# Optimization experiments

Hardware: AMD Instinct MI355X
Metric: run time of the kernel (lower is better)

Reference implementation:

```python
import jax, jax.numpy as jnp
import numpy as np

N, E, D, H, K, G = 100000, 1600000, 64, 64, 3, 64


def setup_inputs() -> dict:
    key = jax.random.key(0)
    ks = jax.random.split(key, 16)
    x = jax.random.normal(ks[0], (N, D), dtype=jnp.float32)
    edge_index = jax.random.randint(ks[1], (2, E), 0, N, dtype=jnp.int64)
    batch = jnp.sort(jax.random.randint(ks[2], (N,), 0, G, dtype=jnp.int64))
    s = 0.1
    inp = {
        "x": x, "edge_index": edge_index, "batch": batch,
        # ChebConv weights: [K, Din, Dout] and bias [Dout]
        "w1": jax.random.normal(ks[3], (K, D, H), dtype=jnp.float32) * s,
        "b1": jnp.zeros((H,), jnp.float32),
        "w2": jax.random.normal(ks[4], (K, H, H), dtype=jnp.float32) * s,
        "b2": jnp.zeros((H,), jnp.float32),
        "w3": jax.random.normal(ks[5], (K, H, H), dtype=jnp.float32) * s,
        "b3": jnp.zeros((H,), jnp.float32),
        # BatchNorm affine params
        "g1": jnp.ones((H,), jnp.float32), "be1": jnp.zeros((H,), jnp.float32),
        "g2": jnp.ones((H,), jnp.float32), "be2": jnp.zeros((H,), jnp.float32),
        "g3": jnp.ones((H,), jnp.float32), "be3": jnp.zeros((H,), jnp.float32),
        # shortcut Linear(input_dim, hidden3) and lin1(hidden3, 1)
        "w_sc": jax.random.normal(ks[6], (D, H), dtype=jnp.float32) * s,
        "b_sc": jnp.zeros((H,), jnp.float32),
        "w_lin": jax.random.normal(ks[7], (H, 1), dtype=jnp.float32) * s,
        "b_lin": jnp.zeros((1,), jnp.float32),
    }
    return inp


def _laplacian_norm(row, col, n):
    # PyG ChebConv default: sym normalization, lambda_max=2 -> L_hat = L - I = -D^{-1/2} A D^{-1/2}
    deg = jax.ops.segment_sum(jnp.ones(row.shape[0], jnp.float32), row, num_segments=n)
    dis = jnp.where(deg > 0, jax.lax.rsqrt(jnp.maximum(deg, 1e-12)), 0.0)
    return -dis[row] * dis[col]  # [E]


def _cheb_conv(x, row, col, norm, W, b):
    n = x.shape[0]
    prop = lambda z: jax.ops.segment_sum(norm[:, None] * z[col], row, num_segments=n)
    Tx0 = x
    out = Tx0 @ W[0]
    Tx1 = prop(Tx0)
    out = out + Tx1 @ W[1]
    for k in range(2, W.shape[0]):
        Tx2 = 2.0 * prop(Tx1) - Tx0
        out = out + Tx2 @ W[k]
        Tx0, Tx1 = Tx1, Tx2
    return out + b


def _bn(x, g, b, eps=1e-5):
    mu = jnp.mean(x, axis=0)
    var = jnp.mean(jnp.square(x - mu), axis=0)  # biased, as torch BN training stats
    return (x - mu) * jax.lax.rsqrt(var + eps) * g + b


def reference(x, edge_index, batch, w1, b1, w2, b2, w3, b3,
              g1, be1, g2, be2, g3, be3, w_sc, b_sc, w_lin, b_lin):
    row, col = edge_index[0], edge_index[1]
    norm = _laplacian_norm(row, col, x.shape[0])
    lrelu = lambda h: jax.nn.leaky_relu(h, negative_slope=0.01)
    identity = x
    h = lrelu(_bn(_cheb_conv(x, row, col, norm, w1, b1), g1, be1))
    h = lrelu(_bn(_cheb_conv(h, row, col, norm, w2, b2), g2, be2))
    h = lrelu(_bn(_cheb_conv(h, row, col, norm, w3, b3), g3, be3))
    h = h + (identity @ w_sc + b_sc)
    pooled = jax.ops.segment_max(h, batch, num_segments=G)  # [G, H]
    return pooled @ w_lin + b_lin  # [G, 1]
```

## Files before the change

### kernel.cpp

```cpp
#include <hip/hip_runtime.h>

#define DIV_UP(a,b) (((a)+(b)-1)/(b))

typedef float v4f __attribute__((ext_vector_type(4)));
typedef unsigned short us4 __attribute__((ext_vector_type(4)));
typedef __attribute__((ext_vector_type(8))) short bf16x8;
typedef __attribute__((ext_vector_type(4))) float f32x4;

__device__ __forceinline__ float4 ntload4(const float* p) {
  v4f v = __builtin_nontemporal_load((const v4f*)p);
  return make_float4(v.x, v.y, v.z, v.w);
}

__device__ __forceinline__ unsigned f2key(float f) {
  unsigned u = __float_as_uint(f);
  return (u & 0x80000000u) ? ~u : (u | 0x80000000u);
}
__device__ __forceinline__ float key2f(unsigned u) {
  unsigned b = (u & 0x80000000u) ? (u ^ 0x80000000u) : ~u;
  return __uint_as_float(b);
}

__device__ __forceinline__ unsigned short f2bf(float f) {
  unsigned u = __float_as_uint(f);
  unsigned r = u + 0x7FFFu + ((u >> 16) & 1u);
  return (unsigned short)(r >> 16);
}
__device__ __forceinline__ float bf2f(unsigned short s) {
  return __uint_as_float(((unsigned)s) << 16);
}

__global__ void k_scan1(const int* __restrict__ cnt, int* __restrict__ incl,
                        int* __restrict__ bsum, int N) {
  __shared__ int s[1024];
  int t = threadIdx.x;
  int i = blockIdx.x * 1024 + t;
  int v = (i < N) ? cnt[i] : 0;
  s[t] = v;
  __syncthreads();
  for (int off = 1; off < 1024; off <<= 1) {
    int add = (t >= off) ? s[t - off] : 0;
    __syncthreads();
    s[t] += add;
    __syncthreads();
  }
  if (i < N) incl[i] = s[t];
  if (t == 1023) bsum[blockIdx.x] = s[1023];
}

__global__ void k_scan2(const int* __restrict__ bsum, int* __restrict__ bex, int nb) {
  __shared__ int s[128];
  int t = threadIdx.x;
  if (nb <= 128) {
    int v = (t < nb) ? bsum[t] : 0;
    s[t] = v;
    __syncthreads();
    for (int off = 1; off < 128; off <<= 1) {
      int add = (t >= off) ? s[t - off] : 0;
      __syncthreads();
      s[t] += add;
      __syncthreads();
    }
    if (t < nb) bex[t] = s[t] - v;
  } else if (t == 0) {
    int run = 0;
    for (int b = 0; b < nb; ++b) { bex[b] = run; run += bsum[b]; }
  }
}

__global__ void k_scan3(const int* __restrict__ incl, const int* __restrict__ cnt,
                        const int* __restrict__ bex, int* __restrict__ rowptr,
                        int* __restrict__ cursor, float* __restrict__ dis,
                        int N, int E) {
  int i = blockIdx.x * blockDim.x + threadIdx.x;
  if (i < N) {
    int c = cnt[i];
    int v = incl[i] - c + bex[i >> 10];
    rowptr[i] = v;
    cursor[i] = v;
    dis[i] = (c > 0) ? rsqrtf((float)c) : 0.0f;
  }
  if (i == 0) rowptr[N] = E;
}

__device__ __forceinline__ void gemmsc_body(unsigned short* wTsc, unsigned short* x16,
                                            int bid,
                                            const float* __restrict__ X,
                                            const float* __restrict__ W,
                                            const float* __restrict__ bias,
                                            unsigned short* __restrict__ Sbf, int N) {
  int tid = threadIdx.x;
  for (int i4 = tid; i4 < 1024; i4 += 512) {
    int d = i4 >> 4, h4 = i4 & 15;
    float4 v = ((const float4*)W)[i4];
    int colb = h4 * 4;
    wTsc[(colb + 0) * 64 + d] = f2bf(v.x);
    wTsc[(colb + 1) * 64 + d] = f2bf(v.y);
    wTsc[(colb + 2) * 64 + d] = f2bf(v.z);
    wTsc[(colb + 3) * 64 + d] = f2bf(v.w);
  }
  int rowbase = bid * 128;
  for (int i4 = tid; i4 < 2048; i4 += 512) {
    int r = i4 >> 4, c4 = i4 & 15;
    int row = rowbase + r;
    float4 v = (row < N) ? ntload4(X + (size_t)row * 64 + c4 * 4)
                         : make_float4(0.f, 0.f, 0.f, 0.f);
    us4 pk;
    pk.x = f2bf(v.x); pk.y = f2bf(v.y); pk.z = f2bf(v.z); pk.w = f2bf(v.w);
    *(us4*)&x16[r * 64 + c4 * 4] = pk;
  }
  __syncthreads();

  int lane = tid & 63;
  int wv = tid >> 6;
  int lo = lane & 15;
  int hi = lane >> 4;

  f32x4 acc[4];
#pragma unroll
  for (int ct = 0; ct < 4; ++ct) acc[ct] = (f32x4){0.f, 0.f, 0.f, 0.f};

#pragma unroll
  for (int ks = 0; ks < 2; ++ks) {
    bf16x8 af = *(const bf16x8*)&x16[(wv * 16 + lo) * 64 + ks * 32 + hi * 8];
#pragma unroll
    for (int ct = 0; ct < 4; ++ct) {
      bf16x8 bfr = *(const bf16x8*)&wTsc[(ct * 16 + lo) * 64 + ks * 32 + hi * 8];
      acc[ct] = __builtin_amdgcn_mfma_f32_16x16x32_bf16(af, bfr, acc[ct], 0, 0, 0);
    }
  }

  float bv[4];
#pragma unroll
  for (int ct = 0; ct < 4; ++ct) bv[ct] = bias[ct * 16 + lo];
  int rowb = rowbase + wv * 16 + hi * 4;
#pragma unroll
  for (int reg = 0; reg < 4; ++reg) {
    int row = rowb + reg;
    if (row < N) {
      size_t o = (size_t)row * 64 + lo;
#pragma unroll
      for (int ct = 0; ct < 4; ++ct)
        __builtin_nontemporal_store(f2bf(acc[ct][reg] + bv[ct]), &Sbf[o + ct * 16]);
    }
  }
}

__device__ __forceinline__ void mfma192_tail(const unsigned short* x16,
                                             const unsigned short* wT,
                                             int rowbase, int tid,
                                             const float* __restrict__ bias,
                                             const float* __restrict__ dis,
                                             unsigned short* __restrict__ A02bf,
                                             unsigned short* __restrict__ Y1bf,
                                             unsigned short* __restrict__ Y2bf,
                                             int N) {
  int lane = tid & 63;
  int wv = tid >> 6;
  int lo = lane & 15;
  int hi = lane >> 4;

  f32x4 acc[12];
#pragma unroll
  for (int ct = 0; ct < 12; ++ct) acc[ct] = (f32x4){0.f, 0.f, 0.f, 0.f};

#pragma unroll
  for (int ks = 0; ks < 2; ++ks) {
    bf16x8 af = *(const bf16x8*)&x16[(wv * 16 + lo) * 64 + ks * 32 + hi * 8];
#pragma unroll
    for (int ct = 0; ct < 12; ++ct) {
      bf16x8 bfr = *(const bf16x8*)&wT[(ct * 16 + lo) * 64 + ks * 32 + hi * 8];
      acc[ct] = __builtin_amdgcn_mfma_f32_16x16x32_bf16(af, bfr, acc[ct], 0, 0, 0);
    }
  }

  float bv[4];
#pragma unroll
  for (int ct = 0; ct < 4; ++ct) bv[ct] = bias[ct * 16 + lo];
  int rowb = rowbase + wv * 16 + hi * 4;
#pragma unroll
  for (int reg = 0; reg < 4; ++reg) {
    int row = rowb + reg;
    if (row < N) {
      float dn = dis[row];
      size_t o = (size_t)row * 64 + lo;
#pragma unroll
      for (int ct = 0; ct < 4; ++ct) {
        float o0 = acc[ct][reg] + bv[ct];
        float o1 = acc[ct + 4][reg];
        float o2 = acc[ct + 8][reg];
        A02bf[o + ct * 16] = f2bf(o0 - o2);
        Y1bf[o + ct * 16] = f2bf(o1);
        Y2bf[o + ct * 16] = f2bf(dn * o2);
      }
    }
  }
}

__device__ __forceinline__ void stage_wT(unsigned short* wT,
                                         const float* __restrict__ W, int tid) {
  for (int i4 = tid; i4 < 3072; i4 += 512) {
    int k3 = i4 >> 10, rem = i4 & 1023;
    int d = rem >> 4, h4 = rem & 15;
    float4 v = ((const float4*)W)[i4];
    int colb = k3 * 64 + h4 * 4;
    wT[(colb + 0) * 64 + d] = f2bf(v.x);
    wT[(colb + 1) * 64 + d] = f2bf(v.y);
    wT[(colb + 2) * 64 + d] = f2bf(v.z);
    wT[(colb + 3) * 64 + d] = f2bf(v.w);
  }
}

__device__ __forceinline__ void gemm192_l0_body(unsigned short* x16, unsigned short* wT,
                                                int bid,
                                                const float* __restrict__ X,
                                                const float* __restrict__ W,
                                                const float* __restrict__ bias,
                                                const float* __restrict__ dis,
                                                unsigned short* __restrict__ A02bf,
                                                unsigned short* __restrict__ Y1bf,
                                                unsigned short* __restrict__ Y2bf,
                                                int N) {
  int tid = threadIdx.x;
  stage_wT(wT, W, tid);
  int rowbase = bid * 128;
  for (int i4 = tid; i4 < 2048; i4 += 512) {
    int r = i4 >> 4, c4 = i4 & 15;
    int row = rowbase + r;
    float4 v = (row < N) ? ntload4(X + (size_t)row * 64 + c4 * 4)
                         : make_float4(0.f, 0.f, 0.f, 0.f);
    us4 pk;
    pk.x = f2bf(v.x); pk.y = f2bf(v.y); pk.z = f2bf(v.z); pk.w = f2bf(v.w);
    *(us4*)&x16[r * 64 + c4 * 4] = pk;
  }
  __syncthreads();
  mfma192_tail(x16, wT, rowbase, tid, bias, dis, A02bf, Y1bf, Y2bf, N);
}

__global__ __launch_bounds__(512) void k_fused_a(const float* __restrict__ X,
                                                 const float* __restrict__ W,
                                                 const float* __restrict__ bias,
                                                 unsigned short* __restrict__ Sbf,
                                                 const int* __restrict__ row,
                                                 int* __restrict__ cnt,
                                                 unsigned short* __restrict__ Y2bf,
                                                 unsigned short* __restrict__ Vbf,
                                                 unsigned* __restrict__ pooled,
                                                 int N, int E, int NBG, int NC,
                                                 int npool, int q) {
  __shared__ unsigned short wTsc[64 * 64];
  __shared__ unsigned short x16a[128 * 64];
  int bid = blockIdx.x;
  bool isg = (bid % q == 0) && (bid / q < NBG);
  if (isg) {
    gemmsc_body(wTsc, x16a, bid / q, X, W, bias, Sbf, N);
  } else {
    int before = min((bid + q - 1) / q, NBG);
    int oi = bid - before;
    if (oi < NC) {
      int e0 = oi * 2048 + threadIdx.x;
      int r[4];
#pragma unroll
      for (int k = 0; k < 4; ++k) {
        int e = e0 + k * 512;
        if (e < E) r[k] = row[e];
      }
#pragma unroll
      for (int k = 0; k < 4; ++k) {
        int e = e0 + k * 512;
        if (e < E) atomicAdd(&cnt[r[k]], 1);
      }
    } else if (oi == NC) {
      if (threadIdx.x < 64) {
        Y2bf[(size_t)N * 64 + threadIdx.x] = 0;
        Vbf[(size_t)N * 64 + threadIdx.x] = 0;
      }
    } else {
      int i = (oi - NC - 1) * 512 + threadIdx.x;
      if (i < npool) pooled[i] = 0x007FFFFFu;
    }
  }
}

__global__ __launch_bounds__(512) void k_fused_b(const float* __restrict__ X,
                                                 const float* __restrict__ W,
                                                 const float* __restrict__ bias,
                                                 const float* __restrict__ dis,
                                                 unsigned short* __restrict__ A02bf,
                                                 unsigned short* __restrict__ Y1bf,
                                                 unsigned short* __restrict__ Y2bf,
                                                 const int* __restrict__ row,
                                                 const int* __restrict__ col,
                                                 int* __restrict__ cursor,
                                                 int* __restrict__ ccol,
                                                 int N, int E, int NBG, int q) {
  __shared__ unsigned short x16b[128 * 64];
  __shared__ unsigned short wTb[192 * 64];
  int bid = blockIdx.x;
  bool isg = (bid % q == 0) && (bid / q < NBG);
  if (isg) {
    gemm192_l0_body(x16b, wTb, bid / q, X, W, bias, dis, A02bf, Y1bf, Y2bf, N);
  } else {
    int before = min((bid + q - 1) / q, NBG);
    int oi = bid - before;
    int e0 = oi * 2048 + threadIdx.x;
    int r[4], c[4], idx[4];
#pragma unroll
    for (int k = 0; k < 4; ++k) {
      int e = e0 + k * 512;
      if (e < E) { r[k] = row[e]; c[k] = col[e]; }
    }
#pragma unroll
    for (int k = 0; k < 4; ++k) {
      int e = e0 + k * 512;
      if (e < E) idx[k] = atomicAdd(&cursor[r[k]], 1);
    }
#pragma unroll
    for (int k = 0; k < 4; ++k) {
      int e = e0 + k * 512;
      if (e < E) ccol[idx[k]] = c[k];
    }
  }
}

__global__ __launch_bounds__(512) void k_gemm192(
    const unsigned short* __restrict__ Cbf,
    const float* __restrict__ sums, const float* __restrict__ sumsq,
    const float* __restrict__ g, const float* __restrict__ be,
    const float* __restrict__ W, const float* __restrict__ bias,
    const float* __restrict__ dis,
    unsigned short* __restrict__ A02bf, unsigned short* __restrict__ Y1bf,
    unsigned short* __restrict__ Y2bf, int N) {
  __shared__ unsigned short x16[128 * 64];
  __shared__ unsigned short wT[192 * 64];
  int bid = blockIdx.x;
  int tid = threadIdx.x;

  int cb = (tid & 15) * 4;
  float inv_n = 1.0f / (float)N;
  float scv[4], shv[4];
#pragma unroll
  for (int k = 0; k < 4; ++k) {
    float mu = sums[cb + k] * inv_n;
    float var = sumsq[cb + k] * inv_n - mu * mu;
    float sc = g[cb + k] * rsqrtf(var + 1e-5f);
    scv[k] = sc;
    shv[k] = be[cb + k] - mu * sc;
  }

  stage_wT(wT, W, tid);

  int rowbase = bid * 128;
  for (int i4 = tid; i4 < 2048; i4 += 512) {
    int r = i4 >> 4, c4 = i4 & 15;
    int row = rowbase + r;
    float vx, vy, vz, vw;
    if (row < N) {
      unsigned long long u =
          *(const unsigned long long*)(Cbf + (size_t)row * 64 + c4 * 4);
      vx = bf2f((unsigned short)(u & 0xffffu));
      vy = bf2f((unsigned short)((u >> 16) & 0xffffu));
      vz = bf2f((unsigned short)((u >> 32) & 0xffffu));
      vw = bf2f((unsigned short)(u >> 48));
    } else {
      vx = vy = vz = vw = 0.f;
    }
    float a = vx * scv[0] + shv[0];
    float b = vy * scv[1] + shv[1];
    float c = vz * scv[2] + shv[2];
    float d = vw * scv[3] + shv[3];
    a = (a > 0.f) ? a : 0.01f * a;
    b = (b > 0.f) ? b : 0.01f * b;
    c = (c > 0.f) ? c : 0.01f * c;
    d = (d > 0.f) ? d : 0.01f * d;
    us4 pk;
    pk.x = f2bf(a); pk.y = f2bf(b); pk.z = f2bf(c); pk.w = f2bf(d);
    *(us4*)&x16[r * 64 + c4 * 4] = pk;
  }
  __syncthreads();

  mfma192_tail(x16, wT, rowbase, tid, bias, dis, A02bf, Y1bf, Y2bf, N);
}

__device__ __forceinline__ void gather4(int cw, int qtr, int s,
                                        const unsigned long long* z64, float* a) {
#pragma unroll
  for (int u = 0; u < 4; ++u) {
    int c = __shfl(cw, 4 * u + qtr, 64);
    unsigned long long zv = z64[(size_t)c * 16 + s];
    unsigned d0 = (unsigned)zv, d1 = (unsigned)(zv >> 32);
    a[0] += __uint_as_float(d0 << 16);
    a[1] += __uint_as_float(d0 & 0xFFFF0000u);
    a[2] += __uint_as_float(d1 << 16);
    a[3] += __uint_as_float(d1 & 0xFFFF0000u);
  }
}

template <int MODE>
__global__ __launch_bounds__(256) void k_prop4(const int* __restrict__ rowptr,
                                               const int* __restrict__ ccol,
                                               const float* __restrict__ dis,
                                               const unsigned short* __restrict__ zbf,
                                               const unsigned short* __restrict__ inAbf,
                                               unsigned short* __restrict__ outbf,
                                               float* __restrict__ sums,
                                               float* __restrict__ sumsq,
                                               float* __restrict__ zstats,
                                               int N, int nwaves) {
  if (MODE == 1 && blockIdx.x == 0 && threadIdx.x < 128) zstats[threadIdx.x] = 0.f;
  int gw = blockIdx.x * 4 + (threadIdx.x >> 6);
  int lane = threadIdx.x & 63;
  int wid = threadIdx.x >> 6;
  int qtr = lane >> 4;
  int s = lane & 15;
  const unsigned long long* z64 = (const unsigned long long*)zbf;
  const unsigned long long* inA64 = (const unsigned long long*)inAbf;
  unsigned long long* out64 = (unsigned long long*)outbf;
  float st[4] = {0.f, 0.f, 0.f, 0.f}, st2[4] = {0.f, 0.f, 0.f, 0.f};

  int n = gw, beg = 0, end = 0, cl = 0;
  if (n < N) {
    beg = rowptr[n];
    end = rowptr[n + 1];
    cl = ccol[beg + s];
  }
  while (n < N) {
    int nn = n + nwaves;
    int begn = 0, endn = 0;
    if (nn < N) {
      begn = rowptr[nn];
      endn = rowptr[nn + 1];
    }
    float dn = dis[n];
    size_t o = (size_t)n * 16 + s;
    unsigned long long av = 0;
    if (qtr == 0) av = inA64[o];
    float a[4] = {0.f, 0.f, 0.f, 0.f};
    {
      int c16 = (beg + s < end) ? cl : N;
      gather4(c16, qtr, s, z64, a);
    }
    for (int j = beg + 16; j < end; j += 16) {
      int jj = j + s;
      int c = ccol[jj];
      c = (jj < end) ? c : N;
      gather4(c, qtr, s, z64, a);
    }
    int cln = 0;
    if (nn < N) cln = ccol[begn + s];
#pragma unroll
    for (int k = 0; k < 4; ++k) {
      a[k] += __shfl_xor(a[k], 16, 64);
      a[k] += __shfl_xor(a[k], 32, 64);
    }
    if (qtr == 0) {
      unsigned b0 = (unsigned)av, b1 = (unsigned)(av >> 32);
      float x0 = __uint_as_float(b0 << 16);
      float x1 = __uint_as_float(b0 & 0xFFFF0000u);
      float x2 = __uint_as_float(b1 << 16);
      float x3 = __uint_as_float(b1 & 0xFFFF0000u);
      if (MODE == 1) {
        float v0 = dn * (x0 - 2.f * dn * a[0]);
        float v1 = dn * (x1 - 2.f * dn * a[1]);
        float v2 = dn * (x2 - 2.f * dn * a[2]);
        float v3 = dn * (x3 - 2.f * dn * a[3]);
        unsigned lo = (unsigned)f2bf(v0) | ((unsigned)f2bf(v1) << 16);
        unsigned hi = (unsigned)f2bf(v2) | ((unsigned)f2bf(v3) << 16);
        out64[o] = (unsigned long long)lo | ((unsigned long long)hi << 32);
      } else {
        float v0 = x0 - dn * a[0];
        float v1 = x1 - dn * a[1];
        float v2 = x2 - dn * a[2];
        float v3 = x3 - dn * a[3];
        unsigned lo = (unsigned)f2bf(v0) | ((unsigned)f2bf(v1) << 16);
        unsigned hi = (unsigned)f2bf(v2) | ((unsigned)f2bf(v3) << 16);
        out64[o] = (unsigned long long)lo | ((unsigned long long)hi << 32);
        st[0] += v0; st2[0] = fmaf(v0, v0, st2[0]);
        st[1] += v1; st2[1] = fmaf(v1, v1, st2[1]);
        st[2] += v2; st2[2] = fmaf(v2, v2, st2[2]);
        st[3] += v3; st2[3] = fmaf(v3, v3, st2[3]);
      }
    }
    n = nn; beg = begn; end = endn; cl = cln;
  }
  if (MODE == 2) {
    __shared__ float red[2][4][64];
    if (qtr == 0) {
#pragma unroll
      for (int k = 0; k < 4; ++k) {
        red[0][wid][4 * s + k] = st[k];
        red[1][wid][4 * s + k] = st2[k];
      }
    }
    __syncthreads();
    if (wid == 0) {
      float a = red[0][0][lane] + red[0][1][lane] + red[0][2][lane] + red[0][3][lane];
      float b = red[1][0][lane] + red[1][1][lane] + red[1][2][lane] + red[1][3][lane];
      atomicAdd(&sums[lane], a);
      atomicAdd(&sumsq[lane], b);
    }
  }
}

__global__ void k_bnpool(const unsigned short* __restrict__ Cbf,
                         const float* __restrict__ sums, const float* __restrict__ sumsq,
                         const float* __restrict__ g, const float* __restrict__ be,
                         const unsigned short* __restrict__ Sbf,
                         const int* __restrict__ batch,
                         unsigned* __restrict__ pooled, int N) {
  __shared__ float sc_s[64], sh_s[64];
  if (threadIdx.x < 64) {
    int h = threadIdx.x;
    float inv_n = 1.0f / (float)N;
    float mu = sums[h] * inv_n;
    float var = sumsq[h] * inv_n - mu * mu;
    float sc = g[h] * rsqrtf(var + 1e-5f);
    sc_s[h] = sc;
    sh_s[h] = be[h] - mu * sc;
  }
  __syncthreads();
  int t = threadIdx.x;
  int h = t & 63;
  int rsub = t >> 6;
  int base = blockIdx.x * 64;
  float sc = sc_s[h], sh = sh_s[h];
  int cur_g = -1;
  unsigned best = 0;
  for (int i = 0; i < 16; ++i) {
    int n = base + rsub + 4 * i;
    if (n >= N) break;
    int gidx = batch[n];
    size_t o = (size_t)n * 64 + h;
    float a = bf2f(__builtin_nontemporal_load(&Cbf[o])) * sc + sh;
    a = (a > 0.f) ? a : 0.01f * a;
    a += bf2f(__builtin_nontemporal_load(&Sbf[o]));
    unsigned k = f2key(a);
    if (gidx != cur_g) {
      if (cur_g >= 0) atomicMax(&pooled[cur_g * 64 + h], best);
      cur_g = gidx;
      best = k;
    } else {
      best = max(best, k);
    }
  }
  if (cur_g >= 0) atomicMax(&pooled[cur_g * 64 + h], best);
}

__global__ void k_final(const unsigned* __restrict__ pooled, const float* __restrict__ w_lin,
                        const float* __restrict__ b_lin, float* __restrict__ out) {
  int g = blockIdx.x;
  int h = threadIdx.x;
  float v = key2f(pooled[g * 64 + h]) * w_lin[h];
  for (int off = 32; off > 0; off >>= 1) v += __shfl_down(v, off, 64);
  if (h == 0) out[g] = v + b_lin[0];
}

extern "C" void kernel_launch(void* const* d_in, const int* in_sizes, int n_in,
                              void* d_out, int out_size, void* d_ws, size_t ws_size,
                              hipStream_t stream) {
  const float* x = (const float*)d_in[0];
  const int* ei = (const int*)d_in[1];
  const int* batch = (const int*)d_in[2];
  const float* w1 = (const float*)d_in[3];
  const float* b1 = (const float*)d_in[4];
  const float* w2 = (const float*)d_in[5];
  const float* b2 = (const float*)d_in[6];
  const float* w3 = (const float*)d_in[7];
  const float* b3 = (const float*)d_in[8];
  const float* g1 = (const float*)d_in[9];
  const float* be1 = (const float*)d_in[10];
  const float* g2 = (const float*)d_in[11];
  const float* be2 = (const float*)d_in[12];
  const float* g3 = (const float*)d_in[13];
  const float* be3 = (const float*)d_in[14];
  const float* w_sc = (const float*)d_in[15];
  const float* b_sc = (const float*)d_in[16];
  const float* w_lin = (const float*)d_in[17];
  const float* b_lin = (const float*)d_in[18];

  int N = in_sizes[0] / 64;
  int E = in_sizes[1] / 2;
  int G = out_size;
  const int* row = ei;
  const int* col = ei + E;

  char* p = (char*)d_ws;
  auto carve = [&](size_t bytes) -> void* {
    void* r = (void*)p;
    p += (bytes + 255) & ~(size_t)255;
    return r;
  };
  int* cnt = (int*)carve((size_t)N * 4);
  float* dis = (float*)carve((size_t)N * 4);
  int* rowptr = (int*)carve((size_t)(N + 1) * 4);
  int* cursor = (int*)carve((size_t)N * 4);
  int* incl = (int*)carve((size_t)N * 4);
  int* bsum = (int*)carve(1024);
  int* bex = (int*)carve(1024);
  int* ccol = (int*)carve((size_t)(E + 64) * 4);
  unsigned short* Sbf = (unsigned short*)carve((size_t)N * 64 * 2);
  unsigned short* A02bf = (unsigned short*)carve((size_t)N * 64 * 2);
  unsigned short* Y1bf = (unsigned short*)carve((size_t)N * 64 * 2);
  unsigned short* Y2bf = (unsigned short*)carve((size_t)(N + 1) * 64 * 2);
  unsigned short* Vbf = (unsigned short*)carve((size_t)(N + 1) * 64 * 2);
  unsigned short* Cbf = (unsigned short*)carve((size_t)N * 64 * 2);
  float* stats = (float*)carve(256 * 4);
  unsigned* pooled = (unsigned*)carve((size_t)G * 64 * 4);

  int NBG = DIV_UP(N, 128);
  int NC = DIV_UP(E, 2048);
  int npool = G * 64;
  int NPI = DIV_UP(npool, 512);

  int TA = NBG + NC + 1 + NPI;
  int qa = (NBG > 1) ? (TA - 1) / (NBG - 1) : 1;
  if (qa < 1) qa = 1;
  int TB = NBG + NC;
  int qb = (NBG > 1) ? (TB - 1) / (NBG - 1) : 1;
  if (qb < 1) qb = 1;

  hipMemsetAsync(cnt, 0, (size_t)N * 4, stream);
  k_fused_a<<<TA, 512, 0, stream>>>(x, w_sc, b_sc, Sbf, row, cnt,
                                    Y2bf, Vbf, pooled, N, E, NBG, NC, npool, qa);
  int nb = DIV_UP(N, 1024);
  k_scan1<<<nb, 1024, 0, stream>>>(cnt, incl, bsum, N);
  k_scan2<<<1, 128, 0, stream>>>(bsum, bex, nb);
  k_scan3<<<DIV_UP(N, 256), 256, 0, stream>>>(incl, cnt, bex, rowptr, cursor, dis, N, E);
  k_fused_b<<<TB, 512, 0, stream>>>(x, w1, b1, dis, A02bf, Y1bf, Y2bf,
                                    row, col, cursor, ccol, N, E, NBG, qb);

  const float* Ws[3] = {w1, w2, w3};
  const float* bs[3] = {b1, b2, b3};
  const float* gs[3] = {g1, g2, g3};
  const float* bes[3] = {be1, be2, be3};

  const int PBLK = 2048;
  const int NWAVE = PBLK * 4;
  for (int l = 0; l < 3; ++l) {
    if (l > 0)
      k_gemm192<<<NBG, 512, 0, stream>>>(Cbf, stats, stats + 64, gs[l - 1], bes[l - 1],
                                         Ws[l], bs[l], dis, A02bf, Y1bf, Y2bf, N);
    k_prop4<1><<<PBLK, 256, 0, stream>>>(rowptr, ccol, dis, Y2bf, Y1bf,
                                         Vbf, nullptr, nullptr, stats, N, NWAVE);
    k_prop4<2><<<PBLK, 256, 0, stream>>>(rowptr, ccol, dis, Vbf, A02bf,
                                         Cbf, stats, stats + 64, nullptr, N, NWAVE);
  }

  k_bnpool<<<DIV_UP(N, 64), 256, 0, stream>>>(Cbf, stats, stats + 64, g3, be3,
                                              Sbf, batch, pooled, N);
  k_final<<<G, 64, 0, stream>>>(pooled, w_lin, b_lin, (float*)d_out);
}
```

Baseline: 646.9 us.

## Swizzle LDS tiles for MFMA loads and record edge slots during counting

Applies an XOR swizzle to the bf16 activation and transposed weight tiles in LDS, on both the staging writes and the MFMA fragment reads, to cut bank conflicts. The CSR build also keeps the return value of the degree-count atomic as a per-edge slot. The scatter pass then places each column at rowptr+slot without a second round of atomics on a cursor array. This costs an extra E-sized int buffer with one store and one load per edge, in exchange for dropping the second atomic pass.

```diff
diff --git a/kernel.cpp b/kernel.cpp
--- a/kernel.cpp
+++ b/kernel.cpp
@@ -28,6 +28,10 @@
 }
 __device__ __forceinline__ float bf2f(unsigned short s) {
   return __uint_as_float(((unsigned)s) << 16);
+}
+
+__device__ __forceinline__ int swz(int row) {
+  return ((row ^ (row >> 3)) & 7) << 3;
 }
 
 __global__ void k_scan1(const int* __restrict__ cnt, int* __restrict__ incl,
@@ -70,14 +74,11 @@
 
 __global__ void k_scan3(const int* __restrict__ incl, const int* __restrict__ cnt,
                         const int* __restrict__ bex, int* __restrict__ rowptr,
-                        int* __restrict__ cursor, float* __restrict__ dis,
-                        int N, int E) {
+                        float* __restrict__ dis, int N, int E) {
   int i = blockIdx.x * blockDim.x + threadIdx.x;
   if (i < N) {
     int c = cnt[i];
-    int v = incl[i] - c + bex[i >> 10];
-    rowptr[i] = v;
-    cursor[i] = v;
+    rowptr[i] = incl[i] - c + bex[i >> 10];
     dis[i] = (c > 0) ? rsqrtf((float)c) : 0.0f;
   }
   if (i == 0) rowptr[N] = E;
@@ -94,10 +95,10 @@
     int d = i4 >> 4, h4 = i4 & 15;
     float4 v = ((const float4*)W)[i4];
     int colb = h4 * 4;
-    wTsc[(colb + 0) * 64 + d] = f2bf(v.x);
-    wTsc[(colb + 1) * 64 + d] = f2bf(v.y);
-    wTsc[(colb + 2) * 64 + d] = f2bf(v.z);
-    wTsc[(colb + 3) * 64 + d] = f2bf(v.w);
+    wTsc[(colb + 0) * 64 + (d ^ swz(colb + 0))] = f2bf(v.x);
+    wTsc[(colb + 1) * 64 + (d ^ swz(colb + 1))] = f2bf(v.y);
+    wTsc[(colb + 2) * 64 + (d ^ swz(colb + 2))] = f2bf(v.z);
+    wTsc[(colb + 3) * 64 + (d ^ swz(colb + 3))] = f2bf(v.w);
   }
   int rowbase = bid * 128;
   for (int i4 = tid; i4 < 2048; i4 += 512) {
@@ -107,7 +108,7 @@
                          : make_float4(0.f, 0.f, 0.f, 0.f);
     us4 pk;
     pk.x = f2bf(v.x); pk.y = f2bf(v.y); pk.z = f2bf(v.z); pk.w = f2bf(v.w);
-    *(us4*)&x16[r * 64 + c4 * 4] = pk;
+    *(us4*)&x16[r * 64 + ((c4 * 4) ^ swz(r))] = pk;
   }
   __syncthreads();
 
@@ -122,10 +123,12 @@
 
 #pragma unroll
   for (int ks = 0; ks < 2; ++ks) {
-    bf16x8 af = *(const bf16x8*)&x16[(wv * 16 + lo) * 64 + ks * 32 + hi * 8];
+    int ar = wv * 16 + lo;
+    bf16x8 af = *(const bf16x8*)&x16[ar * 64 + ((ks * 32 + hi * 8) ^ swz(ar))];
 #pragma unroll
     for (int ct = 0; ct < 4; ++ct) {
-      bf16x8 bfr = *(const bf16x8*)&wTsc[(ct * 16 + lo) * 64 + ks * 32 + hi * 8];
+      int br = ct * 16 + lo;
+      bf16x8 bfr = *(const bf16x8*)&wTsc[br * 64 + ((ks * 32 + hi * 8) ^ swz(br))];
       acc[ct] = __builtin_amdgcn_mfma_f32_16x16x32_bf16(af, bfr, acc[ct], 0, 0, 0);
     }
   }
@@ -166,10 +169,12 @@
 
 #pragma unroll
   for (int ks = 0; ks < 2; ++ks) {
-    bf16x8 af = *(const bf16x8*)&x16[(wv * 16 + lo) * 64 + ks * 32 + hi * 8];
+    int ar = wv * 16 + lo;
+    bf16x8 af = *(const bf16x8*)&x16[ar * 64 + ((ks * 32 + hi * 8) ^ swz(ar))];
 #pragma unroll
     for (int ct = 0; ct < 12; ++ct) {
-      bf16x8 bfr = *(const bf16x8*)&wT[(ct * 16 + lo) * 64 + ks * 32 + hi * 8];
+      int br = ct * 16 + lo;
+      bf16x8 bfr = *(const bf16x8*)&wT[br * 64 + ((ks * 32 + hi * 8) ^ swz(br))];
       acc[ct] = __builtin_amdgcn_mfma_f32_16x16x32_bf16(af, bfr, acc[ct], 0, 0, 0);
     }
   }
@@ -204,10 +209,10 @@
     int d = rem >> 4, h4 = rem & 15;
     float4 v = ((const float4*)W)[i4];
     int colb = k3 * 64 + h4 * 4;
-    wT[(colb + 0) * 64 + d] = f2bf(v.x);
-    wT[(colb + 1) * 64 + d] = f2bf(v.y);
-    wT[(colb + 2) * 64 + d] = f2bf(v.z);
-    wT[(colb + 3) * 64 + d] = f2bf(v.w);
+    wT[(colb + 0) * 64 + (d ^ swz(colb + 0))] = f2bf(v.x);
+    wT[(colb + 1) * 64 + (d ^ swz(colb + 1))] = f2bf(v.y);
+    wT[(colb + 2) * 64 + (d ^ swz(colb + 2))] = f2bf(v.z);
+    wT[(colb + 3) * 64 + (d ^ swz(colb + 3))] = f2bf(v.w);
   }
 }
 
@@ -231,7 +236,7 @@
                          : make_float4(0.f, 0.f, 0.f, 0.f);
     us4 pk;
     pk.x = f2bf(v.x); pk.y = f2bf(v.y); pk.z = f2bf(v.z); pk.w = f2bf(v.w);
-    *(us4*)&x16[r * 64 + c4 * 4] = pk;
+    *(us4*)&x16[r * 64 + ((c4 * 4) ^ swz(r))] = pk;
   }
   __syncthreads();
   mfma192_tail(x16, wT, rowbase, tid, bias, dis, A02bf, Y1bf, Y2bf, N);
@@ -243,6 +248,7 @@
                                                  unsigned short* __restrict__ Sbf,
                                                  const int* __restrict__ row,
                                                  int* __restrict__ cnt,
+                                                 int* __restrict__ eslot,
                                                  unsigned short* __restrict__ Y2bf,
                                                  unsigned short* __restrict__ Vbf,
                                                  unsigned* __restrict__ pooled,
@@ -259,7 +265,7 @@
     int oi = bid - before;
     if (oi < NC) {
       int e0 = oi * 2048 + threadIdx.x;
-      int r[4];
+      int r[4], idx[4];
 #pragma unroll
       for (int k = 0; k < 4; ++k) {
         int e = e0 + k * 512;
@@ -268,7 +274,12 @@
 #pragma unroll
       for (int k = 0; k < 4; ++k) {
         int e = e0 + k * 512;
-        if (e < E) atomicAdd(&cnt[r[k]], 1);
+        if (e < E) idx[k] = atomicAdd(&cnt[r[k]], 1);
+      }
+#pragma unroll
+      for (int k = 0; k < 4; ++k) {
+        int e = e0 + k * 512;
+        if (e < E) __builtin_nontemporal_store(idx[k], &eslot[e]);
       }
     } else if (oi == NC) {
       if (threadIdx.x < 64) {
@@ -291,7 +302,8 @@
                                                  unsigned short* __restrict__ Y2bf,
                                                  const int* __restrict__ row,
                                                  const int* __restrict__ col,
-                                                 int* __restrict__ cursor,
+                                                 const int* __restrict__ rowptr,
+                                                 const int* __restrict__ eslot,
                                                  int* __restrict__ ccol,
                                                  int N, int E, int NBG, int q) {
   __shared__ unsigned short x16b[128 * 64];
@@ -304,21 +316,21 @@
     int before = min((bid + q - 1) / q, NBG);
     int oi = bid - before;
     int e0 = oi * 2048 + threadIdx.x;
-    int r[4], c[4], idx[4];
+    int r[4], c[4], sl[4], base[4];
 #pragma unroll
     for (int k = 0; k < 4; ++k) {
       int e = e0 + k * 512;
-      if (e < E) { r[k] = row[e]; c[k] = col[e]; }
+      if (e < E) { r[k] = row[e]; c[k] = col[e]; sl[k] = eslot[e]; }
     }
 #pragma unroll
     for (int k = 0; k < 4; ++k) {
       int e = e0 + k * 512;
-      if (e < E) idx[k] = atomicAdd(&cursor[r[k]], 1);
+      if (e < E) base[k] = rowptr[r[k]];
     }
 #pragma unroll
     for (int k = 0; k < 4; ++k) {
       int e = e0 + k * 512;
-      if (e < E) ccol[idx[k]] = c[k];
+      if (e < E) ccol[base[k] + sl[k]] = c[k];
     }
   }
 }
@@ -375,7 +387,7 @@
     d = (d > 0.f) ? d : 0.01f * d;
     us4 pk;
     pk.x = f2bf(a); pk.y = f2bf(b); pk.z = f2bf(c); pk.w = f2bf(d);
-    *(us4*)&x16[r * 64 + c4 * 4] = pk;
+    *(us4*)&x16[r * 64 + ((c4 * 4) ^ swz(r))] = pk;
   }
   __syncthreads();
 
@@ -593,7 +605,7 @@
   int* cnt = (int*)carve((size_t)N * 4);
   float* dis = (float*)carve((size_t)N * 4);
   int* rowptr = (int*)carve((size_t)(N + 1) * 4);
-  int* cursor = (int*)carve((size_t)N * 4);
+  int* eslot = (int*)carve((size_t)E * 4);
   int* incl = (int*)carve((size_t)N * 4);
   int* bsum = (int*)carve(1024);
   int* bex = (int*)carve(1024);
@@ -620,14 +632,14 @@
   if (qb < 1) qb = 1;
 
   hipMemsetAsync(cnt, 0, (size_t)N * 4, stream);
-  k_fused_a<<<TA, 512, 0, stream>>>(x, w_sc, b_sc, Sbf, row, cnt,
+  k_fused_a<<<TA, 512, 0, stream>>>(x, w_sc, b_sc, Sbf, row, cnt, eslot,
                                     Y2bf, Vbf, pooled, N, E, NBG, NC, npool, qa);
   int nb = DIV_UP(N, 1024);
   k_scan1<<<nb, 1024, 0, stream>>>(cnt, incl, bsum, N);
   k_scan2<<<1, 128, 0, stream>>>(bsum, bex, nb);
-  k_scan3<<<DIV_UP(N, 256), 256, 0, stream>>>(incl, cnt, bex, rowptr, cursor, dis, N, E);
+  k_scan3<<<DIV_UP(N, 256), 256, 0, stream>>>(incl, cnt, bex, rowptr, dis, N, E);
   k_fused_b<<<TB, 512, 0, stream>>>(x, w1, b1, dis, A02bf, Y1bf, Y2bf,
-                                    row, col, cursor, ccol, N, E, NBG, qb);
+                                    row, col, rowptr, eslot, ccol, N, E, NBG, qb);
 
   const float* Ws[3] = {w1, w2, w3};
   const float* bs[3] = {b1, b2, b3};
```

Measured after the change: 628.3 us. 1.03x faster.
